# Kernel optimization log

Measured on AMD Instinct MI355X. Metric: run time of the kernel, lower is better.

Reference implementation:

```python
import jax, jax.numpy as jnp
import numpy as np

N = 100_000      # nodes
E = 1_600_000    # edges (avg degree 16)
F_IN = 165       # Elliptic node features
HID = 64         # hidden_units
NCLS = 2         # num_classes
NEG_SLOPE = 0.2  # PyG GATConv default


def setup_inputs() -> dict:
    key = jax.random.key(0)
    ks = jax.random.split(key, 9)
    x = jax.random.normal(ks[0], (N, F_IN), jnp.float32)
    edge_index = jax.random.randint(ks[1], (2, E), 0, N, jnp.int32)
    W1 = jax.random.normal(ks[2], (F_IN, HID), jnp.float32) / np.sqrt(F_IN)
    a1_src = jax.random.normal(ks[3], (HID,), jnp.float32) / np.sqrt(HID)
    a1_dst = jax.random.normal(ks[4], (HID,), jnp.float32) / np.sqrt(HID)
    b1 = jnp.zeros((HID,), jnp.float32)
    W2 = jax.random.normal(ks[5], (HID, NCLS), jnp.float32) / np.sqrt(HID)
    a2_src = jax.random.normal(ks[6], (NCLS,), jnp.float32) / np.sqrt(NCLS)
    a2_dst = jax.random.normal(ks[7], (NCLS,), jnp.float32) / np.sqrt(NCLS)
    b2 = jnp.zeros((NCLS,), jnp.float32)
    return {"x": x, "edge_index": edge_index, "W1": W1, "a1_src": a1_src,
            "a1_dst": a1_dst, "b1": b1, "W2": W2, "a2_src": a2_src,
            "a2_dst": a2_dst, "b2": b2}


def gat_layer(x, src, dst, W, a_s, a_d, b, n):
    # h: [N, out]; per-edge attention e_ij = LeakyReLU(a_s.h_j + a_d.h_i)
    h = x @ W
    e = jax.nn.leaky_relu((h @ a_s)[src] + (h @ a_d)[dst], NEG_SLOPE)
    # numerically stable segment softmax over incoming edges of each dst node
    emax = jax.ops.segment_max(e, dst, num_segments=n)
    ee = jnp.exp(e - jax.lax.stop_gradient(emax)[dst])
    denom = jax.ops.segment_sum(ee, dst, num_segments=n)
    alpha = ee / denom[dst]                       # [E_tot]
    out = jax.ops.segment_sum(alpha[:, None] * h[src], dst, num_segments=n)
    return out + b


def reference(x, edge_index, W1, a1_src, a1_dst, b1, W2, a2_src, a2_dst, b2):
    n = x.shape[0]
    loops = jnp.arange(n, dtype=edge_index.dtype)   # PyG add_self_loops=True
    src = jnp.concatenate([edge_index[0], loops])
    dst = jnp.concatenate([edge_index[1], loops])
    h = jax.nn.relu(gat_layer(x, src, dst, W1, a1_src, a1_dst, b1, n))
    # F.dropout(training=False) is identity in eval mode
    out = gat_layer(h, src, dst, W2, a2_src, a2_dst, b2, n)
    return out, edge_index
```

## Files before the change

kernel.cpp:

```cpp
#include <hip/hip_runtime.h>
#include <hip/hip_bf16.h>
#include <math.h>

#define N_NODES 100000
#define N_EDGES 1600000
#define F_IN 165
#define HID 64
#define SLOPE 0.2f

#define NBUCK 196
#define BSHIFT 9
#define BMASK 511
#define NBLK 256
#define CHUNK 6250
#define MSCAN (NBUCK * NBLK)

typedef short short8 __attribute__((ext_vector_type(8)));
typedef float f32x4 __attribute__((ext_vector_type(4)));
typedef float f32x2 __attribute__((ext_vector_type(2)));

__device__ __forceinline__ float lrelu(float x) { return x > 0.f ? x : SLOPE * x; }

__device__ __forceinline__ unsigned short f2bf(float f) {
    unsigned u = __float_as_uint(f);
    u += 0x7FFFu + ((u >> 16) & 1u);
    return (unsigned short)(u >> 16);
}
__device__ __forceinline__ unsigned char f2fp8(float f) {
    return (unsigned char)(__builtin_amdgcn_cvt_pk_fp8_f32(f, f, 0, false) & 0xFF);
}

__global__ void k_wsw(const float* __restrict__ W1, unsigned short* __restrict__ Wsw) {
    int idx = blockIdx.x * 256 + threadIdx.x;
    if (idx >= 12288) return;
    int j = idx & 7;
    int r = idx >> 3;
    int n = r & 15; r >>= 4;
    int t = r & 3;  r >>= 2;
    int q = r & 3;  int c = r >> 2;
    int k = c * 32 + q * 8 + j;
    int col = t * 16 + n;
    float v = (k < F_IN) ? W1[k * HID + col] : 0.f;
    Wsw[idx] = f2bf(v);
}

#define ASTRIDE 200
__global__ __launch_bounds__(256, 4) void k_gemm1(const float* __restrict__ x,
                                                  const unsigned short* __restrict__ Wsw,
                                                  const float* __restrict__ a1s,
                                                  const float* __restrict__ a1d,
                                                  unsigned char* __restrict__ h1,
                                                  float* __restrict__ s1,
                                                  float* __restrict__ d1) {
    __shared__ unsigned short Ah[64 * ASTRIDE];
    const int tid = threadIdx.x;
    const int base = blockIdx.x * 64;

    for (int i = tid; i < 64 * 35; i += 256) {
        int nl = i / 35, kk = 165 + (i - nl * 35);
        Ah[nl * ASTRIDE + kk] = 0;
    }
    const int fbase = base * F_IN;
    const int flim = N_NODES * F_IN;
    for (int i = tid; i < (64 * F_IN) / 4; i += 256) {
        int f = fbase + i * 4;
        float vv[4];
        if (f + 4 <= flim) {
            float4 v = *(const float4*)&x[f];
            vv[0] = v.x; vv[1] = v.y; vv[2] = v.z; vv[3] = v.w;
        } else {
#pragma unroll
            for (int e = 0; e < 4; e++) vv[e] = (f + e < flim) ? x[f + e] : 0.f;
        }
#pragma unroll
        for (int e = 0; e < 4; e++) {
            int g = f + e;
            int node = g / F_IN;
            int kk = g - node * F_IN;
            Ah[(node - base) * ASTRIDE + kk] = f2bf(vv[e]);
        }
    }
    __syncthreads();

    const int lane = tid & 63;
    const int w = tid >> 6;
    const int m16 = lane & 15;
    const int q = lane >> 4;
    f32x4 acc[4];
#pragma unroll
    for (int t = 0; t < 4; t++) acc[t] = (f32x4){0.f, 0.f, 0.f, 0.f};

    const unsigned short* arow = &Ah[(w * 16 + m16) * ASTRIDE];
    const short8* Wsw8 = (const short8*)Wsw;
#pragma unroll
    for (int c = 0; c < 6; c++) {
        short8 a = *(const short8*)&arow[c * 32 + q * 8];
#pragma unroll
        for (int t = 0; t < 4; t++) {
            short8 b = Wsw8[(c * 4 + q) * 64 + t * 16 + m16];
            acc[t] = __builtin_amdgcn_mfma_f32_16x16x32_bf16(a, b, acc[t], 0, 0, 0);
        }
    }

    float as_l[4], ad_l[4];
#pragma unroll
    for (int t = 0; t < 4; t++) { as_l[t] = a1s[t * 16 + m16]; ad_l[t] = a1d[t * 16 + m16]; }
#pragma unroll
    for (int r = 0; r < 4; r++) {
        int node = base + w * 16 + q * 4 + r;
        bool ok = node < N_NODES;
        float ps = 0.f, pd = 0.f;
#pragma unroll
        for (int t = 0; t < 4; t++) {
            float v = acc[t][r];
            if (ok) h1[(size_t)node * HID + t * 16 + m16] = f2fp8(v);
            ps += v * as_l[t];
            pd += v * ad_l[t];
        }
#pragma unroll
        for (int off = 1; off < 16; off <<= 1) {
            ps += __shfl_xor(ps, off);
            pd += __shfl_xor(pd, off);
        }
        if (ok && m16 == 0) { s1[node] = ps; d1[node] = pd; }
    }
}

__global__ __launch_bounds__(256) void k_hist(const int* __restrict__ ei,
                                              int* __restrict__ hist,
                                              float* __restrict__ out_edges) {
    __shared__ int h[NBUCK];
    int blk = blockIdx.x, t = threadIdx.x;
    for (int j = t; j < NBUCK; j += 256) h[j] = 0;
    __syncthreads();
    int i0 = blk * CHUNK, i1 = i0 + CHUNK;
    for (int i = i0 + t; i < i1; i += 256) {
        int s = ei[i];
        int d = ei[N_EDGES + i];
        out_edges[i] = (float)s;
        out_edges[N_EDGES + i] = (float)d;
        atomicAdd(&h[d >> BSHIFT], 1);
    }
    __syncthreads();
    for (int j = t; j < NBUCK; j += 256) hist[j * NBLK + blk] = h[j];
}

__global__ void k_scan1(int* __restrict__ a, int* __restrict__ bsum) {
    __shared__ int sd[256];
    int i = blockIdx.x * 256 + threadIdx.x;
    int v = a[i];
    sd[threadIdx.x] = v;
    __syncthreads();
    for (int off = 1; off < 256; off <<= 1) {
        int t = (threadIdx.x >= off) ? sd[threadIdx.x - off] : 0;
        __syncthreads();
        sd[threadIdx.x] += t;
        __syncthreads();
    }
    a[i] = sd[threadIdx.x] - v;
    if (threadIdx.x == 255) bsum[blockIdx.x] = sd[255];
}

__global__ void k_scan2(int* __restrict__ bsum, int nb) {
    __shared__ int sd[256];
    int t = threadIdx.x;
    int v = (t < nb) ? bsum[t] : 0;
    sd[t] = v;
    __syncthreads();
    for (int off = 1; off < 256; off <<= 1) {
        int u = (t >= off) ? sd[t - off] : 0;
        __syncthreads();
        sd[t] += u;
        __syncthreads();
    }
    if (t < nb) bsum[t] = sd[t] - v;
}

__global__ void k_scan3(int* __restrict__ a, const int* __restrict__ bsum) {
    int i = blockIdx.x * 256 + threadIdx.x;
    a[i] += bsum[blockIdx.x];
}

__global__ __launch_bounds__(256) void k_part(const int* __restrict__ ei,
                                              const int* __restrict__ off,
                                              unsigned* __restrict__ pairs) {
    __shared__ int base_s[NBUCK];
    __shared__ int cnt[NBUCK];
    int blk = blockIdx.x, t = threadIdx.x;
    for (int j = t; j < NBUCK; j += 256) {
        base_s[j] = off[j * NBLK + blk];
        cnt[j] = 0;
    }
    __syncthreads();
    int i0 = blk * CHUNK, i1 = i0 + CHUNK;
    for (int i = i0 + t; i < i1; i += 256) {
        int s = ei[i];
        int d = ei[N_EDGES + i];
        int b = d >> BSHIFT;
        int pos = base_s[b] + atomicAdd(&cnt[b], 1);
        pairs[pos] = ((unsigned)s << BSHIFT) | (unsigned)(d & BMASK);
    }
}

__global__ __launch_bounds__(512) void k_build2(const unsigned* __restrict__ pairs,
                                                const int* __restrict__ off,
                                                int* __restrict__ row_ptr,
                                                int* __restrict__ deg,
                                                int* __restrict__ csr) {
    __shared__ int hcnt[512];
    __shared__ int cur[512];
    int b = blockIdx.x, t = threadIdx.x;
    hcnt[t] = 0;
    __syncthreads();
    int rs = off[b * NBLK];
    int re = (b == NBUCK - 1) ? N_EDGES : off[(b + 1) * NBLK];
    for (int j = rs + t; j < re; j += 512)
        atomicAdd(&hcnt[pairs[j] & BMASK], 1);
    __syncthreads();
    int v = hcnt[t];
    cur[t] = v;
    __syncthreads();
    for (int o = 1; o < 512; o <<= 1) {
        int u = (t >= o) ? cur[t - o] : 0;
        __syncthreads();
        cur[t] += u;
        __syncthreads();
    }
    int excl = cur[t] - v;
    __syncthreads();
    cur[t] = rs + excl;
    int node = b * 512 + t;
    if (node < N_NODES) {
        row_ptr[node] = rs + excl;
        deg[node] = v;
    }
    __syncthreads();
    for (int j = rs + t; j < re; j += 512) {
        unsigned p = pairs[j];
        int pos = atomicAdd(&cur[p & BMASK], 1);
        csr[pos] = (int)(p >> BSHIFT);
    }
}

__global__ __launch_bounds__(256) void k_agg1(const unsigned char* __restrict__ h1,
                                              const float* __restrict__ s1,
                                              const float* __restrict__ d1,
                                              const int* __restrict__ row_ptr,
                                              const int* __restrict__ deg,
                                              const int* __restrict__ csr,
                                              const float* __restrict__ b1,
                                              const float* __restrict__ W2,
                                              const float* __restrict__ a2s,
                                              const float* __restrict__ a2d,
                                              float* __restrict__ node2) {
    int wid = (blockIdx.x * blockDim.x + threadIdx.x) >> 6;
    int lane = threadIdx.x & 63;
    if (wid >= N_NODES) return;
    int slot = lane >> 4;
    int cg = lane & 15;
    float di = d1[wid];
    float dpart = 0.f;
    float4 acc = make_float4(0.f, 0.f, 0.f, 0.f);
    int rs = row_ptr[wid], re = rs + deg[wid];
    for (int b = rs; b < re; b += 64) {
        int j = b + lane;
        int srcl = 0;
        float eel = 0.f;
        if (j < re) {
            srcl = csr[j];
            eel = __expf(lrelu(s1[srcl] + di));
        }
        int tmax = min(16, (re - b + 3) >> 2);
        for (int t = 0; t < tmax; t++) {
            int s = __shfl(srcl, t * 4 + slot);
            float ee = __shfl(eel, t * 4 + slot);
            unsigned u = *(const unsigned*)&h1[((size_t)s << 6) + cg * 4];
            f32x2 lo = __builtin_amdgcn_cvt_pk_f32_fp8((int)u, false);
            f32x2 hi = __builtin_amdgcn_cvt_pk_f32_fp8((int)u, true);
            dpart += ee;
            acc.x += ee * lo.x; acc.y += ee * lo.y;
            acc.z += ee * hi.x; acc.w += ee * hi.y;
        }
    }
#pragma unroll
    for (int off = 16; off < 64; off <<= 1) {
        acc.x += __shfl_xor(acc.x, off);
        acc.y += __shfl_xor(acc.y, off);
        acc.z += __shfl_xor(acc.z, off);
        acc.w += __shfl_xor(acc.w, off);
        dpart += __shfl_xor(dpart, off);
    }
    float ees = __expf(lrelu(s1[wid] + di));
    unsigned us = *(const unsigned*)&h1[((size_t)wid << 6) + cg * 4];
    f32x2 slo = __builtin_amdgcn_cvt_pk_f32_fp8((int)us, false);
    f32x2 shi = __builtin_amdgcn_cvt_pk_f32_fp8((int)us, true);
    float denom = dpart + ees;
    acc.x += ees * slo.x; acc.y += ees * slo.y;
    acc.z += ees * shi.x; acc.w += ees * shi.y;
    float inv = 1.f / denom;
    float4 bb = *(const float4*)&b1[cg * 4];
    float o0 = fmaxf(acc.x * inv + bb.x, 0.f);
    float o1 = fmaxf(acc.y * inv + bb.y, 0.f);
    float o2 = fmaxf(acc.z * inv + bb.z, 0.f);
    float o3 = fmaxf(acc.w * inv + bb.w, 0.f);
    float2 w0 = *(const float2*)&W2[(cg * 4 + 0) * 2];
    float2 w1 = *(const float2*)&W2[(cg * 4 + 1) * 2];
    float2 w2 = *(const float2*)&W2[(cg * 4 + 2) * 2];
    float2 w3 = *(const float2*)&W2[(cg * 4 + 3) * 2];
    float p0 = o0 * w0.x + o1 * w1.x + o2 * w2.x + o3 * w3.x;
    float p1 = o0 * w0.y + o1 * w1.y + o2 * w2.y + o3 * w3.y;
#pragma unroll
    for (int off = 1; off < 16; off <<= 1) {
        p0 += __shfl_xor(p0, off);
        p1 += __shfl_xor(p1, off);
    }
    if (lane == 0) {
        float s2 = p0 * a2s[0] + p1 * a2s[1];
        float d2 = p0 * a2d[0] + p1 * a2d[1];
        *(float4*)&node2[(size_t)wid * 4] = make_float4(p0, p1, s2, d2);
    }
}

__global__ __launch_bounds__(256) void k_agg2(const float* __restrict__ node2,
                                              const int* __restrict__ row_ptr,
                                              const int* __restrict__ deg,
                                              const int* __restrict__ csr,
                                              const float* __restrict__ b2,
                                              float* __restrict__ out) {
    int wid = (blockIdx.x * blockDim.x + threadIdx.x) >> 6;
    int lane = threadIdx.x & 63;
    int node = wid * 4 + (lane >> 4);
    int eg = lane & 15;
    if (node >= N_NODES) return;
    float4 vi = *(const float4*)&node2[(size_t)node * 4];
    float d2 = vi.w;
    float denom = 0.f, p0 = 0.f, p1 = 0.f;
    int rs = row_ptr[node], re = rs + deg[node];
    for (int j = rs + eg; j < re; j += 16) {
        int s = csr[j];
        float4 v = *(const float4*)&node2[(size_t)s * 4];
        float ee = __expf(lrelu(v.z + d2));
        denom += ee;
        p0 += ee * v.x;
        p1 += ee * v.y;
    }
#pragma unroll
    for (int off = 1; off < 16; off <<= 1) {
        denom += __shfl_xor(denom, off);
        p0 += __shfl_xor(p0, off);
        p1 += __shfl_xor(p1, off);
    }
    if (eg == 0) {
        float ee = __expf(lrelu(vi.z + d2));
        denom += ee;
        p0 += ee * vi.x;
        p1 += ee * vi.y;
        out[(size_t)node * 2 + 0] = p0 / denom + b2[0];
        out[(size_t)node * 2 + 1] = p1 / denom + b2[1];
    }
}

extern "C" void kernel_launch(void* const* d_in, const int* in_sizes, int n_in,
                              void* d_out, int out_size, void* d_ws, size_t ws_size,
                              hipStream_t stream) {
    const float* x   = (const float*)d_in[0];
    const int*   ei  = (const int*)d_in[1];
    const float* W1  = (const float*)d_in[2];
    const float* a1s = (const float*)d_in[3];
    const float* a1d = (const float*)d_in[4];
    const float* b1  = (const float*)d_in[5];
    const float* W2  = (const float*)d_in[6];
    const float* a2s = (const float*)d_in[7];
    const float* a2d = (const float*)d_in[8];
    const float* b2  = (const float*)d_in[9];
    float* out = (float*)d_out;

    unsigned char* h1 = (unsigned char*)d_ws;
    float* s1      = (float*)(h1 + (size_t)N_NODES * HID);
    float* d1      = s1 + N_NODES;
    float* node2   = d1 + N_NODES;
    int* row_ptr   = (int*)(node2 + (size_t)N_NODES * 4);
    int* deg       = row_ptr + N_NODES;
    int* off       = deg + N_NODES;
    int* bsum      = off + MSCAN + 64;
    int* csr       = bsum + 256;
    unsigned* pairs = (unsigned*)(csr + N_EDGES);
    unsigned short* Wsw = (unsigned short*)(pairs + N_EDGES);

    k_wsw<<<48, 256, 0, stream>>>(W1, Wsw);
    k_hist<<<NBLK, 256, 0, stream>>>(ei, off, out + 2 * N_NODES);
    k_gemm1<<<(N_NODES + 63) / 64, 256, 0, stream>>>(x, Wsw, a1s, a1d, h1, s1, d1);
    k_scan1<<<MSCAN / 256, 256, 0, stream>>>(off, bsum);
    k_scan2<<<1, 256, 0, stream>>>(bsum, MSCAN / 256);
    k_scan3<<<MSCAN / 256, 256, 0, stream>>>(off, bsum);
    k_part<<<NBLK, 256, 0, stream>>>(ei, off, pairs);
    k_build2<<<NBUCK, 512, 0, stream>>>(pairs, off, row_ptr, deg, csr);
    k_agg1<<<N_NODES / 4, 256, 0, stream>>>(h1, s1, d1, row_ptr, deg, csr,
                                            b1, W2, a2s, a2d, node2);
    k_agg2<<<(N_NODES + 15) / 16, 256, 0, stream>>>(node2, row_ptr, deg, csr, b2, out);
}
```

Baseline: 247.5 us.

## Fuse weight swizzle and scan fixup, vectorize edge reads, pack layer-2 node data

Merges the W1 swizzle into the histogram kernel and drops the scan add-back kernel by applying block sums where the offsets are consumed, cutting two launches. Edge-index reads in the histogram and partition kernels become int2 loads. The layer-1 aggregation gather is unrolled four-wide to keep more loads in flight, and its occupancy hint is raised. Layer-2 node features are packed as bf16 with fp32 score into 8 bytes to halve gather traffic, at some precision cost.

```diff
diff --git a/kernel.cpp b/kernel.cpp
--- a/kernel.cpp
+++ b/kernel.cpp
@@ -26,22 +26,44 @@
     u += 0x7FFFu + ((u >> 16) & 1u);
     return (unsigned short)(u >> 16);
 }
+__device__ __forceinline__ float bflo(unsigned u) { return __uint_as_float(u << 16); }
+__device__ __forceinline__ float bfhi(unsigned u) { return __uint_as_float(u & 0xFFFF0000u); }
 __device__ __forceinline__ unsigned char f2fp8(float f) {
     return (unsigned char)(__builtin_amdgcn_cvt_pk_fp8_f32(f, f, 0, false) & 0xFF);
 }
 
-__global__ void k_wsw(const float* __restrict__ W1, unsigned short* __restrict__ Wsw) {
-    int idx = blockIdx.x * 256 + threadIdx.x;
-    if (idx >= 12288) return;
-    int j = idx & 7;
-    int r = idx >> 3;
-    int n = r & 15; r >>= 4;
-    int t = r & 3;  r >>= 2;
-    int q = r & 3;  int c = r >> 2;
-    int k = c * 32 + q * 8 + j;
-    int col = t * 16 + n;
-    float v = (k < F_IN) ? W1[k * HID + col] : 0.f;
-    Wsw[idx] = f2bf(v);
+__global__ __launch_bounds__(256) void k_hist(const int* __restrict__ ei,
+                                              int* __restrict__ hist,
+                                              float* __restrict__ out_edges,
+                                              const float* __restrict__ W1,
+                                              unsigned short* __restrict__ Wsw) {
+    int blk = blockIdx.x, t = threadIdx.x;
+    int idx = blk * 256 + t;
+    if (idx < 12288) {
+        int j = idx & 7;
+        int r = idx >> 3;
+        int n = r & 15; r >>= 4;
+        int tt = r & 3; r >>= 2;
+        int q = r & 3;  int c = r >> 2;
+        int k = c * 32 + q * 8 + j;
+        int col = tt * 16 + n;
+        float v = (k < F_IN) ? W1[k * HID + col] : 0.f;
+        Wsw[idx] = f2bf(v);
+    }
+    __shared__ int h[NBUCK];
+    for (int j = t; j < NBUCK; j += 256) h[j] = 0;
+    __syncthreads();
+    int i0 = blk * CHUNK, i1 = i0 + CHUNK;
+    for (int i = i0 + t * 2; i < i1; i += 512) {
+        int2 sv = *(const int2*)&ei[i];
+        int2 dv = *(const int2*)&ei[N_EDGES + i];
+        *(float2*)&out_edges[i] = make_float2((float)sv.x, (float)sv.y);
+        *(float2*)&out_edges[N_EDGES + i] = make_float2((float)dv.x, (float)dv.y);
+        atomicAdd(&h[dv.x >> BSHIFT], 1);
+        atomicAdd(&h[dv.y >> BSHIFT], 1);
+    }
+    __syncthreads();
+    for (int j = t; j < NBUCK; j += 256) hist[j * NBLK + blk] = h[j];
 }
 
 #define ASTRIDE 200
@@ -126,25 +148,6 @@
     }
 }
 
-__global__ __launch_bounds__(256) void k_hist(const int* __restrict__ ei,
-                                              int* __restrict__ hist,
-                                              float* __restrict__ out_edges) {
-    __shared__ int h[NBUCK];
-    int blk = blockIdx.x, t = threadIdx.x;
-    for (int j = t; j < NBUCK; j += 256) h[j] = 0;
-    __syncthreads();
-    int i0 = blk * CHUNK, i1 = i0 + CHUNK;
-    for (int i = i0 + t; i < i1; i += 256) {
-        int s = ei[i];
-        int d = ei[N_EDGES + i];
-        out_edges[i] = (float)s;
-        out_edges[N_EDGES + i] = (float)d;
-        atomicAdd(&h[d >> BSHIFT], 1);
-    }
-    __syncthreads();
-    for (int j = t; j < NBUCK; j += 256) hist[j * NBLK + blk] = h[j];
-}
-
 __global__ void k_scan1(int* __restrict__ a, int* __restrict__ bsum) {
     __shared__ int sd[256];
     int i = blockIdx.x * 256 + threadIdx.x;
@@ -176,34 +179,34 @@
     if (t < nb) bsum[t] = sd[t] - v;
 }
 
-__global__ void k_scan3(int* __restrict__ a, const int* __restrict__ bsum) {
-    int i = blockIdx.x * 256 + threadIdx.x;
-    a[i] += bsum[blockIdx.x];
-}
-
 __global__ __launch_bounds__(256) void k_part(const int* __restrict__ ei,
                                               const int* __restrict__ off,
+                                              const int* __restrict__ bsum,
                                               unsigned* __restrict__ pairs) {
     __shared__ int base_s[NBUCK];
     __shared__ int cnt[NBUCK];
     int blk = blockIdx.x, t = threadIdx.x;
     for (int j = t; j < NBUCK; j += 256) {
-        base_s[j] = off[j * NBLK + blk];
+        base_s[j] = off[j * NBLK + blk] + bsum[j];
         cnt[j] = 0;
     }
     __syncthreads();
     int i0 = blk * CHUNK, i1 = i0 + CHUNK;
-    for (int i = i0 + t; i < i1; i += 256) {
-        int s = ei[i];
-        int d = ei[N_EDGES + i];
-        int b = d >> BSHIFT;
-        int pos = base_s[b] + atomicAdd(&cnt[b], 1);
-        pairs[pos] = ((unsigned)s << BSHIFT) | (unsigned)(d & BMASK);
+    for (int i = i0 + t * 2; i < i1; i += 512) {
+        int2 sv = *(const int2*)&ei[i];
+        int2 dv = *(const int2*)&ei[N_EDGES + i];
+        int b0 = dv.x >> BSHIFT;
+        int p0 = base_s[b0] + atomicAdd(&cnt[b0], 1);
+        pairs[p0] = ((unsigned)sv.x << BSHIFT) | (unsigned)(dv.x & BMASK);
+        int b1v = dv.y >> BSHIFT;
+        int p1 = base_s[b1v] + atomicAdd(&cnt[b1v], 1);
+        pairs[p1] = ((unsigned)sv.y << BSHIFT) | (unsigned)(dv.y & BMASK);
     }
 }
 
 __global__ __launch_bounds__(512) void k_build2(const unsigned* __restrict__ pairs,
                                                 const int* __restrict__ off,
+                                                const int* __restrict__ bsum,
                                                 int* __restrict__ row_ptr,
                                                 int* __restrict__ deg,
                                                 int* __restrict__ csr) {
@@ -212,8 +215,8 @@
     int b = blockIdx.x, t = threadIdx.x;
     hcnt[t] = 0;
     __syncthreads();
-    int rs = off[b * NBLK];
-    int re = (b == NBUCK - 1) ? N_EDGES : off[(b + 1) * NBLK];
+    int rs = off[b * NBLK] + bsum[b];
+    int re = (b == NBUCK - 1) ? N_EDGES : off[(b + 1) * NBLK] + bsum[b + 1];
     for (int j = rs + t; j < re; j += 512)
         atomicAdd(&hcnt[pairs[j] & BMASK], 1);
     __syncthreads();
@@ -242,17 +245,18 @@
     }
 }
 
-__global__ __launch_bounds__(256) void k_agg1(const unsigned char* __restrict__ h1,
-                                              const float* __restrict__ s1,
-                                              const float* __restrict__ d1,
-                                              const int* __restrict__ row_ptr,
-                                              const int* __restrict__ deg,
-                                              const int* __restrict__ csr,
-                                              const float* __restrict__ b1,
-                                              const float* __restrict__ W2,
-                                              const float* __restrict__ a2s,
-                                              const float* __restrict__ a2d,
-                                              float* __restrict__ node2) {
+__global__ __launch_bounds__(256, 8) void k_agg1(const unsigned char* __restrict__ h1,
+                                                 const float* __restrict__ s1,
+                                                 const float* __restrict__ d1,
+                                                 const int* __restrict__ row_ptr,
+                                                 const int* __restrict__ deg,
+                                                 const int* __restrict__ csr,
+                                                 const float* __restrict__ b1,
+                                                 const float* __restrict__ W2,
+                                                 const float* __restrict__ a2s,
+                                                 const float* __restrict__ a2d,
+                                                 uint2* __restrict__ node2,
+                                                 float* __restrict__ d2arr) {
     int wid = (blockIdx.x * blockDim.x + threadIdx.x) >> 6;
     int lane = threadIdx.x & 63;
     if (wid >= N_NODES) return;
@@ -270,16 +274,50 @@
             srcl = csr[j];
             eel = __expf(lrelu(s1[srcl] + di));
         }
-        int tmax = min(16, (re - b + 3) >> 2);
-        for (int t = 0; t < tmax; t++) {
-            int s = __shfl(srcl, t * 4 + slot);
-            float ee = __shfl(eel, t * 4 + slot);
-            unsigned u = *(const unsigned*)&h1[((size_t)s << 6) + cg * 4];
-            f32x2 lo = __builtin_amdgcn_cvt_pk_f32_fp8((int)u, false);
-            f32x2 hi = __builtin_amdgcn_cvt_pk_f32_fp8((int)u, true);
-            dpart += ee;
-            acc.x += ee * lo.x; acc.y += ee * lo.y;
-            acc.z += ee * hi.x; acc.w += ee * hi.y;
+        int cnt = re - b; if (cnt > 64) cnt = 64;
+        int tmax = (cnt + 3) >> 2;
+        for (int t = 0; t < tmax; t += 4) {
+            int n = tmax - t; if (n > 4) n = 4;
+            int s0 = 0, s1i = 0, s2i = 0, s3i = 0;
+            float e0 = 0.f, e1 = 0.f, e2 = 0.f, e3 = 0.f;
+            s0 = __shfl(srcl, (t + 0) * 4 + slot);
+            e0 = __shfl(eel, (t + 0) * 4 + slot);
+            if (n > 1) { s1i = __shfl(srcl, (t + 1) * 4 + slot); e1 = __shfl(eel, (t + 1) * 4 + slot); }
+            if (n > 2) { s2i = __shfl(srcl, (t + 2) * 4 + slot); e2 = __shfl(eel, (t + 2) * 4 + slot); }
+            if (n > 3) { s3i = __shfl(srcl, (t + 3) * 4 + slot); e3 = __shfl(eel, (t + 3) * 4 + slot); }
+            unsigned u0 = 0, u1 = 0, u2 = 0, u3 = 0;
+            u0 = *(const unsigned*)&h1[((size_t)s0 << 6) + cg * 4];
+            if (n > 1) u1 = *(const unsigned*)&h1[((size_t)s1i << 6) + cg * 4];
+            if (n > 2) u2 = *(const unsigned*)&h1[((size_t)s2i << 6) + cg * 4];
+            if (n > 3) u3 = *(const unsigned*)&h1[((size_t)s3i << 6) + cg * 4];
+            {
+                f32x2 lo = __builtin_amdgcn_cvt_pk_f32_fp8((int)u0, false);
+                f32x2 hi = __builtin_amdgcn_cvt_pk_f32_fp8((int)u0, true);
+                dpart += e0;
+                acc.x += e0 * lo.x; acc.y += e0 * lo.y;
+                acc.z += e0 * hi.x; acc.w += e0 * hi.y;
+            }
+            if (n > 1) {
+                f32x2 lo = __builtin_amdgcn_cvt_pk_f32_fp8((int)u1, false);
+                f32x2 hi = __builtin_amdgcn_cvt_pk_f32_fp8((int)u1, true);
+                dpart += e1;
+                acc.x += e1 * lo.x; acc.y += e1 * lo.y;
+                acc.z += e1 * hi.x; acc.w += e1 * hi.y;
+            }
+            if (n > 2) {
+                f32x2 lo = __builtin_amdgcn_cvt_pk_f32_fp8((int)u2, false);
+                f32x2 hi = __builtin_amdgcn_cvt_pk_f32_fp8((int)u2, true);
+                dpart += e2;
+                acc.x += e2 * lo.x; acc.y += e2 * lo.y;
+                acc.z += e2 * hi.x; acc.w += e2 * hi.y;
+            }
+            if (n > 3) {
+                f32x2 lo = __builtin_amdgcn_cvt_pk_f32_fp8((int)u3, false);
+                f32x2 hi = __builtin_amdgcn_cvt_pk_f32_fp8((int)u3, true);
+                dpart += e3;
+                acc.x += e3 * lo.x; acc.y += e3 * lo.y;
+                acc.z += e3 * hi.x; acc.w += e3 * hi.y;
+            }
         }
     }
 #pragma unroll
@@ -316,12 +354,15 @@
     }
     if (lane == 0) {
         float s2 = p0 * a2s[0] + p1 * a2s[1];
-        float d2 = p0 * a2d[0] + p1 * a2d[1];
-        *(float4*)&node2[(size_t)wid * 4] = make_float4(p0, p1, s2, d2);
-    }
-}
-
-__global__ __launch_bounds__(256) void k_agg2(const float* __restrict__ node2,
+        float d2v = p0 * a2d[0] + p1 * a2d[1];
+        unsigned pk = (unsigned)f2bf(p0) | ((unsigned)f2bf(p1) << 16);
+        node2[wid] = make_uint2(pk, __float_as_uint(s2));
+        d2arr[wid] = d2v;
+    }
+}
+
+__global__ __launch_bounds__(256) void k_agg2(const uint2* __restrict__ node2,
+                                              const float* __restrict__ d2arr,
                                               const int* __restrict__ row_ptr,
                                               const int* __restrict__ deg,
                                               const int* __restrict__ csr,
@@ -332,17 +373,17 @@
     int node = wid * 4 + (lane >> 4);
     int eg = lane & 15;
     if (node >= N_NODES) return;
-    float4 vi = *(const float4*)&node2[(size_t)node * 4];
-    float d2 = vi.w;
+    uint2 vi = node2[node];
+    float d2 = d2arr[node];
     float denom = 0.f, p0 = 0.f, p1 = 0.f;
     int rs = row_ptr[node], re = rs + deg[node];
     for (int j = rs + eg; j < re; j += 16) {
         int s = csr[j];
-        float4 v = *(const float4*)&node2[(size_t)s * 4];
-        float ee = __expf(lrelu(v.z + d2));
+        uint2 v = node2[s];
+        float ee = __expf(lrelu(__uint_as_float(v.y) + d2));
         denom += ee;
-        p0 += ee * v.x;
-        p1 += ee * v.y;
+        p0 += ee * bflo(v.x);
+        p1 += ee * bfhi(v.x);
     }
 #pragma unroll
     for (int off = 1; off < 16; off <<= 1) {
@@ -351,10 +392,10 @@
         p1 += __shfl_xor(p1, off);
     }
     if (eg == 0) {
-        float ee = __expf(lrelu(vi.z + d2));
+        float ee = __expf(lrelu(__uint_as_float(vi.y) + d2));
         denom += ee;
-        p0 += ee * vi.x;
-        p1 += ee * vi.y;
+        p0 += ee * bflo(vi.x);
+        p1 += ee * bfhi(vi.x);
         out[(size_t)node * 2 + 0] = p0 / denom + b2[0];
         out[(size_t)node * 2 + 1] = p1 / denom + b2[1];
     }
@@ -378,8 +419,9 @@
     unsigned char* h1 = (unsigned char*)d_ws;
     float* s1      = (float*)(h1 + (size_t)N_NODES * HID);
     float* d1      = s1 + N_NODES;
-    float* node2   = d1 + N_NODES;
-    int* row_ptr   = (int*)(node2 + (size_t)N_NODES * 4);
+    float* d2arr   = d1 + N_NODES;
+    uint2* node2   = (uint2*)(d2arr + N_NODES);
+    int* row_ptr   = (int*)(node2 + N_NODES);
     int* deg       = row_ptr + N_NODES;
     int* off       = deg + N_NODES;
     int* bsum      = off + MSCAN + 64;
@@ -387,15 +429,13 @@
     unsigned* pairs = (unsigned*)(csr + N_EDGES);
     unsigned short* Wsw = (unsigned short*)(pairs + N_EDGES);
 
-    k_wsw<<<48, 256, 0, stream>>>(W1, Wsw);
-    k_hist<<<NBLK, 256, 0, stream>>>(ei, off, out + 2 * N_NODES);
+    k_hist<<<NBLK, 256, 0, stream>>>(ei, off, out + 2 * N_NODES, W1, Wsw);
     k_gemm1<<<(N_NODES + 63) / 64, 256, 0, stream>>>(x, Wsw, a1s, a1d, h1, s1, d1);
     k_scan1<<<MSCAN / 256, 256, 0, stream>>>(off, bsum);
     k_scan2<<<1, 256, 0, stream>>>(bsum, MSCAN / 256);
-    k_scan3<<<MSCAN / 256, 256, 0, stream>>>(off, bsum);
-    k_part<<<NBLK, 256, 0, stream>>>(ei, off, pairs);
-    k_build2<<<NBUCK, 512, 0, stream>>>(pairs, off, row_ptr, deg, csr);
+    k_part<<<NBLK, 256, 0, stream>>>(ei, off, bsum, pairs);
+    k_build2<<<NBUCK, 512, 0, stream>>>(pairs, off, bsum, row_ptr, deg, csr);
     k_agg1<<<N_NODES / 4, 256, 0, stream>>>(h1, s1, d1, row_ptr, deg, csr,
-                                            b1, W2, a2s, a2d, node2);
-    k_agg2<<<(N_NODES + 15) / 16, 256, 0, stream>>>(node2, row_ptr, deg, csr, b2, out);
-}
+                                            b1, W2, a2s, a2d, node2, d2arr);
+    k_agg2<<<(N_NODES + 15) / 16, 256, 0, stream>>>(node2, d2arr, row_ptr, deg, csr, b2, out);
+}
```

Result: faster. 229.2 us (-7.4%).
